# Kernel optimization log

Measured on AMD Instinct MI355X. Metric: run time of the kernel, lower is better.

## Reference

```python
import jax, jax.numpy as jnp
import numpy as np

B, T, D, H = 2, 2048, 1024, 16
HD = D // H  # head dim = 64; rope half-dim = 32


def setup_inputs() -> dict:
    key = jax.random.key(0)
    ks = jax.random.split(key, 8)
    x = jax.random.normal(ks[0], (B, T, D), dtype=jnp.float32)
    # additive causal mask (upper triangle = -inf-like), as typically passed in
    mask = jnp.triu(jnp.full((T, T), -1e9, dtype=jnp.float32), k=1)
    # standard RoPE angles: theta = pos / 10000^(2i/hd)
    inv_freq = 1.0 / (10000.0 ** (np.arange(0, HD, 2, dtype=np.float32) / HD))
    ang = np.arange(T, dtype=np.float32)[:, None] * inv_freq[None, :]  # [T, HD//2]
    cos = jnp.asarray(np.cos(ang), dtype=jnp.float32)
    sin = jnp.asarray(np.sin(ang), dtype=jnp.float32)
    s = 1.0 / np.sqrt(D)
    Wq = jax.random.normal(ks[1], (D, D), dtype=jnp.float32) * s
    bq = jnp.zeros((D,), dtype=jnp.float32)
    Wk = jax.random.normal(ks[2], (D, D), dtype=jnp.float32) * s
    Wv = jax.random.normal(ks[3], (D, D), dtype=jnp.float32) * s
    bv = jnp.zeros((D,), dtype=jnp.float32)
    Wo = jax.random.normal(ks[4], (D, D), dtype=jnp.float32) * s
    bo = jnp.zeros((D,), dtype=jnp.float32)
    return {"x": x, "mask": mask, "cos": cos, "sin": sin, "Wq": Wq, "bq": bq,
            "Wk": Wk, "Wv": Wv, "bv": bv, "Wo": Wo, "bo": bo}


def _apply_rope(t, cos, sin):
    # t: [B, T, H, HD]; cos/sin: [T, HD//2]; complex multiply on (even, odd) pairs
    t = t.reshape(B, T, H, HD // 2, 2)
    t0, t1 = t[..., 0], t[..., 1]
    c = cos[None, :, None, :]
    s = sin[None, :, None, :]
    out = jnp.stack([t0 * c - t1 * s, t0 * s + t1 * c], axis=-1)
    return out.reshape(B, T, H, HD)


def reference(x, mask, cos, sin, Wq, bq, Wk, Wv, bv, Wo, bo):
    scale = float(HD) ** (-0.25)
    q = (x @ Wq.T + bq).reshape(B, T, H, HD)
    k = (x @ Wk.T).reshape(B, T, H, HD)  # key proj has no bias
    v = (x @ Wv.T + bv).reshape(B, T, H, HD)
    q = _apply_rope(q, cos, sin)
    k = _apply_rope(k, cos, sin)
    q = q.transpose(0, 2, 1, 3) * scale  # [B,H,T,HD]
    k = k.transpose(0, 2, 1, 3) * scale
    v = v.transpose(0, 2, 1, 3)
    qk = jnp.einsum("bhtd,bhsd->bhts", q, k) + mask  # [B,H,T,T]
    qk = qk.astype(jnp.float32)
    w = jax.nn.softmax(qk, axis=-1).astype(q.dtype)
    wv = jnp.einsum("bhts,bhsd->bhtd", w, v)
    wv = wv.transpose(0, 2, 1, 3).reshape(B, T, D)
    out = wv @ Wo.T + bo
    return out, qk
```

## Files before the change

### kernel.cpp

```cpp
#include <hip/hip_runtime.h>
#include <math.h>

#define Tc 2048
#define Dc 1024
#define Hc 16
#define HDc 64
#define BT 4096
#define SCALE 0.35355339059327379f

typedef _Float16 f16;
typedef __attribute__((ext_vector_type(4))) _Float16 f16x4;
typedef __attribute__((ext_vector_type(8))) _Float16 f16x8;
typedef __attribute__((ext_vector_type(4))) float f32x4;

__device__ __forceinline__ void gload16(const f16* g, f16* l)
{
    __builtin_amdgcn_global_load_lds(
        (const __attribute__((address_space(1))) void*)g,
        (__attribute__((address_space(3))) void*)l, 16, 0, 0);
}

__global__ __launch_bounds__(256)
void cast_kernel(const float* __restrict__ x,
                 const float* __restrict__ Wq, const float* __restrict__ Wk,
                 const float* __restrict__ Wv, const float* __restrict__ Wo,
                 f16* __restrict__ xh,
                 f16* __restrict__ Wqh, f16* __restrict__ Wkh,
                 f16* __restrict__ Wvh, f16* __restrict__ Woh)
{
    const int u = blockIdx.y;
    const float* s; f16* d;
    if (u < 4) { s = x + (size_t)u * (1u << 20); d = xh + (size_t)u * (1u << 20); }
    else switch (u) {
        case 4:  s = Wq; d = Wqh; break;
        case 5:  s = Wk; d = Wkh; break;
        case 6:  s = Wv; d = Wvh; break;
        default: s = Wo; d = Woh; break;
    }
    int i = blockIdx.x * 256 + threadIdx.x;
    float4 v = ((const float4*)s)[i];
    f16x4 o = {(f16)v.x, (f16)v.y, (f16)v.z, (f16)v.w};
    ((f16x4*)d)[i] = o;
}

#define GEMM_BODY(Aptr, Bptr)                                                        \
    __shared__ f16 As[128][64];                                                      \
    __shared__ f16 Bs[128][64];                                                      \
    const int tid = threadIdx.x;                                                     \
    const int w = tid >> 6, l = tid & 63;                                            \
    const int lr = l & 15, lq = l >> 4;                                              \
    const int wr = w >> 1, wc = w & 1;                                               \
    const int m0 = blockIdx.y * 128, n0 = blockIdx.x * 128;                          \
    const int srow8 = l >> 3, sslot = l & 7;                                         \
    f32x4 acc[4][4] = {};                                                            \
    for (int k0 = 0; k0 < Dc; k0 += 64) {                                            \
        __syncthreads();                                                             \
        _Pragma("unroll")                                                            \
        for (int c = 0; c < 4; c++) {                                                \
            int chunk = w * 4 + c;                                                   \
            int row = chunk * 8 + srow8;                                             \
            int col = (sslot ^ (row & 7)) * 8;                                       \
            gload16(&Aptr[(size_t)(m0 + row) * Dc + k0 + col],                       \
                    (f16*)((char*)&As[0][0] + chunk * 1024));                        \
            gload16(&Bptr[(size_t)(n0 + row) * Dc + k0 + col],                       \
                    (f16*)((char*)&Bs[0][0] + chunk * 1024));                        \
        }                                                                            \
        __syncthreads();                                                             \
        _Pragma("unroll")                                                            \
        for (int kk = 0; kk < 2; kk++) {                                             \
            f16x8 af[4], bf[4];                                                      \
            _Pragma("unroll")                                                        \
            for (int mi = 0; mi < 4; mi++) {                                         \
                int row = 64 * wr + 16 * mi + lr;                                    \
                int bo = (lq * 16 + kk * 64) ^ ((row & 7) << 4);                     \
                af[mi] = *(const f16x8*)((const char*)&As[0][0] + row * 128 + bo);   \
            }                                                                        \
            _Pragma("unroll")                                                        \
            for (int ni = 0; ni < 4; ni++) {                                         \
                int row = 64 * wc + 16 * ni + lr;                                    \
                int bo = (lq * 16 + kk * 64) ^ ((row & 7) << 4);                     \
                bf[ni] = *(const f16x8*)((const char*)&Bs[0][0] + row * 128 + bo);   \
            }                                                                        \
            _Pragma("unroll")                                                        \
            for (int mi = 0; mi < 4; mi++)                                           \
                _Pragma("unroll")                                                    \
                for (int ni = 0; ni < 4; ni++)                                       \
                    acc[mi][ni] = __builtin_amdgcn_mfma_f32_16x16x32_f16(            \
                        af[mi], bf[ni], acc[mi][ni], 0, 0, 0);                       \
        }                                                                            \
    }

__global__ __launch_bounds__(256)
void qkv_proj_kernel(const f16* __restrict__ xh,
                     const f16* __restrict__ Wqh, const f16* __restrict__ Wkh,
                     const f16* __restrict__ Wvh,
                     const float* __restrict__ bq, const float* __restrict__ bv,
                     f16* __restrict__ qh, f16* __restrict__ kh, f16* __restrict__ vh,
                     const float* __restrict__ cosp, const float* __restrict__ sinp)
{
    const int mode = blockIdx.z;
    const f16* W = (mode == 0) ? Wqh : (mode == 1 ? Wkh : Wvh);
    const float* bias = (mode == 0) ? bq : (mode == 2 ? bv : nullptr);
    f16* dst = (mode == 0) ? qh : (mode == 1 ? kh : vh);

    GEMM_BODY(xh, W)

    #pragma unroll
    for (int mi = 0; mi < 4; mi++) {
        #pragma unroll
        for (int ni = 0; ni < 4; ni++) {
            #pragma unroll
            for (int i = 0; i < 4; i++) {
                int gm = m0 + 64 * wr + 16 * mi + lq * 4 + i;
                int gn = n0 + 64 * wc + 16 * ni + lr;
                float v = acc[mi][ni][i];
                if (bias) v += bias[gn];
                int b = gm >> 11, t = gm & 2047;
                int h = gn >> 6, d = gn & 63;
                if (mode != 2) {
                    float pv = __shfl_xor(v, 1, 64);
                    int p = d >> 1;
                    float c = cosp[t * 32 + p], s = sinp[t * 32 + p];
                    v = (d & 1) ? (pv * s + v * c) : (v * c - pv * s);
                    v *= SCALE;
                }
                dst[((size_t)(b * Hc + h) * Tc + t) * HDc + d] = (f16)v;
            }
        }
    }
}

__global__ __launch_bounds__(256)
void out_proj_kernel(const f16* __restrict__ A, const f16* __restrict__ W,
                     const float* __restrict__ bias, float* __restrict__ out)
{
    GEMM_BODY(A, W)

    #pragma unroll
    for (int mi = 0; mi < 4; mi++)
        #pragma unroll
        for (int ni = 0; ni < 4; ni++)
            #pragma unroll
            for (int i = 0; i < 4; i++) {
                int gm = m0 + 64 * wr + 16 * mi + lq * 4 + i;
                int gn = n0 + 64 * wc + 16 * ni + lr;
                out[(size_t)gm * Dc + gn] = acc[mi][ni][i] + bias[gn];
            }
}

__global__ __launch_bounds__(256)
void flash_kernel(const f16* __restrict__ qh, const f16* __restrict__ kh,
                  const f16* __restrict__ vh, f16* __restrict__ wvh,
                  float* __restrict__ qk)
{
    const int z = blockIdx.y;
    const int t0 = (gridDim.x - 1 - blockIdx.x) * 64;
    const int tid = threadIdx.x;
    const int w = tid >> 6, l = tid & 63;
    const int lr = l & 15, lq = l >> 4;

    __shared__ f16 Ks[64][72];
    __shared__ f16 VsT[64][72];
    __shared__ f16 Ps[64][72];

    const f16* Qg = qh + (size_t)z * Tc * HDc;
    const f16* Kg = kh + (size_t)z * Tc * HDc;
    const f16* Vg = vh + (size_t)z * Tc * HDc;
    float* C = qk + (size_t)z * Tc * Tc;

    f16x8 aq[2];
    #pragma unroll
    for (int ks = 0; ks < 2; ks++)
        aq[ks] = *(const f16x8*)&Qg[(size_t)(t0 + 16 * w + lr) * HDc + lq * 8 + 32 * ks];

    {
        int r = t0 + (tid >> 2);
        int n4 = (Tc - t0 - 64) >> 2;
        float4 mv; mv.x = mv.y = mv.z = mv.w = -1e9f;
        float4* rowp = (float4*)(C + (size_t)r * Tc + t0 + 64);
        for (int c = (tid & 3); c < n4; c += 4) rowp[c] = mv;
    }

    const int kr = tid >> 2, kc = (tid & 3) * 16;
    const int vs = tid & 63, vd = (tid >> 6) * 16;
    f16x8 rk0 = *(const f16x8*)&Kg[(size_t)kr * HDc + kc];
    f16x8 rk1 = *(const f16x8*)&Kg[(size_t)kr * HDc + kc + 8];
    f16x8 rv0 = *(const f16x8*)&Vg[(size_t)vs * HDc + vd];
    f16x8 rv1 = *(const f16x8*)&Vg[(size_t)vs * HDc + vd + 8];

    f32x4 O[4] = {};
    float mrow[4], lrow[4];
    #pragma unroll
    for (int i = 0; i < 4; i++) { mrow[i] = -1e30f; lrow[i] = 0.f; }

    for (int s0 = 0; s0 <= t0; s0 += 64) {
        asm volatile("" ::: "memory");
        __builtin_amdgcn_s_barrier();
        asm volatile("" ::: "memory");

        *(f16x8*)&Ks[kr][kc]     = rk0;
        *(f16x8*)&Ks[kr][kc + 8] = rk1;
        #pragma unroll
        for (int j = 0; j < 8; j++) {
            VsT[vd + j][vs]     = rv0[j];
            VsT[vd + 8 + j][vs] = rv1[j];
        }

        if (s0 + 64 <= t0) {
            const f16* kp = &Kg[(size_t)(s0 + 64 + kr) * HDc + kc];
            const f16* vp = &Vg[(size_t)(s0 + 64 + vs) * HDc + vd];
            rk0 = *(const f16x8*)kp;
            rk1 = *(const f16x8*)(kp + 8);
            rv0 = *(const f16x8*)vp;
            rv1 = *(const f16x8*)(vp + 8);
        }

        asm volatile("s_waitcnt lgkmcnt(0)" ::: "memory");
        __builtin_amdgcn_s_barrier();
        asm volatile("" ::: "memory");

        f32x4 S[4] = {};
        __builtin_amdgcn_s_setprio(1);
        #pragma unroll
        for (int ks = 0; ks < 2; ks++) {
            #pragma unroll
            for (int ni = 0; ni < 4; ni++) {
                f16x8 bk = *(const f16x8*)&Ks[16 * ni + lr][lq * 8 + 32 * ks];
                S[ni] = __builtin_amdgcn_mfma_f32_16x16x32_f16(aq[ks], bk, S[ni], 0, 0, 0);
            }
        }
        __builtin_amdgcn_s_setprio(0);

        if (s0 == t0) {
            #pragma unroll
            for (int ni = 0; ni < 4; ni++)
                #pragma unroll
                for (int i = 0; i < 4; i++) {
                    int tg = t0 + 16 * w + lq * 4 + i;
                    int sg = s0 + 16 * ni + lr;
                    if (sg > tg) S[ni][i] = -1e9f;
                }
        }

        #pragma unroll
        for (int ni = 0; ni < 4; ni++)
            #pragma unroll
            for (int i = 0; i < 4; i++) {
                int tg = t0 + 16 * w + lq * 4 + i;
                int sg = s0 + 16 * ni + lr;
                C[(size_t)tg * Tc + sg] = S[ni][i];
            }

        #pragma unroll
        for (int i = 0; i < 4; i++) {
            float v = fmaxf(fmaxf(S[0][i], S[1][i]), fmaxf(S[2][i], S[3][i]));
            v = fmaxf(v, __shfl_xor(v, 1, 64));
            v = fmaxf(v, __shfl_xor(v, 2, 64));
            v = fmaxf(v, __shfl_xor(v, 4, 64));
            v = fmaxf(v, __shfl_xor(v, 8, 64));
            float mnew = fmaxf(mrow[i], v);
            float alpha = __expf(mrow[i] - mnew);
            mrow[i] = mnew;
            float rs = 0.f;
            #pragma unroll
            for (int ni = 0; ni < 4; ni++) {
                float p = __expf(S[ni][i] - mnew);
                S[ni][i] = p;
                rs += p;
            }
            rs += __shfl_xor(rs, 1, 64);
            rs += __shfl_xor(rs, 2, 64);
            rs += __shfl_xor(rs, 4, 64);
            rs += __shfl_xor(rs, 8, 64);
            lrow[i] = lrow[i] * alpha + rs;
            #pragma unroll
            for (int ni = 0; ni < 4; ni++) O[ni][i] *= alpha;
        }

        #pragma unroll
        for (int ni = 0; ni < 4; ni++)
            #pragma unroll
            for (int i = 0; i < 4; i++)
                Ps[16 * w + lq * 4 + i][16 * ni + lr] = (f16)S[ni][i];

        __builtin_amdgcn_s_setprio(1);
        #pragma unroll
        for (int ks = 0; ks < 2; ks++) {
            f16x8 ap = *(const f16x8*)&Ps[16 * w + lr][lq * 8 + 32 * ks];
            #pragma unroll
            for (int ni = 0; ni < 4; ni++) {
                f16x8 bv = *(const f16x8*)&VsT[16 * ni + lr][lq * 8 + 32 * ks];
                O[ni] = __builtin_amdgcn_mfma_f32_16x16x32_f16(ap, bv, O[ni], 0, 0, 0);
            }
        }
        __builtin_amdgcn_s_setprio(0);
    }

    const int b = z >> 4, h = z & 15;
    #pragma unroll
    for (int ni = 0; ni < 4; ni++)
        #pragma unroll
        for (int i = 0; i < 4; i++) {
            int tg = t0 + 16 * w + lq * 4 + i;
            int d = 16 * ni + lr;
            float o = O[ni][i] / lrow[i];
            wvh[((size_t)(b * Tc + tg)) * Dc + h * HDc + d] = (f16)o;
        }
}

extern "C" void kernel_launch(void* const* d_in, const int* in_sizes, int n_in,
                              void* d_out, int out_size, void* d_ws, size_t ws_size,
                              hipStream_t stream)
{
    const float* x    = (const float*)d_in[0];
    const float* cosp = (const float*)d_in[2];
    const float* sinp = (const float*)d_in[3];
    const float* Wq   = (const float*)d_in[4];
    const float* bq   = (const float*)d_in[5];
    const float* Wk   = (const float*)d_in[6];
    const float* Wv   = (const float*)d_in[7];
    const float* bv   = (const float*)d_in[8];
    const float* Wo   = (const float*)d_in[9];
    const float* bo   = (const float*)d_in[10];

    float* out = (float*)d_out;
    float* qk  = out + (size_t)BT * Dc;

    f16* ws  = (f16*)d_ws;
    f16* xh  = ws;
    f16* Wqh = xh  + (size_t)BT * Dc;
    f16* Wkh = Wqh + (size_t)Dc * Dc;
    f16* Wvh = Wkh + (size_t)Dc * Dc;
    f16* Woh = Wvh + (size_t)Dc * Dc;
    f16* qh  = Woh + (size_t)Dc * Dc;
    f16* kh  = qh  + (size_t)BT * Dc;
    f16* vh  = kh  + (size_t)BT * Dc;
    f16* wvh = vh  + (size_t)BT * Dc;

    dim3 blk(256);

    cast_kernel<<<dim3(1024, 8), blk, 0, stream>>>(
        x, Wq, Wk, Wv, Wo, xh, Wqh, Wkh, Wvh, Woh);

    qkv_proj_kernel<<<dim3(Dc / 128, BT / 128, 3), blk, 0, stream>>>(
        xh, Wqh, Wkh, Wvh, bq, bv, qh, kh, vh, cosp, sinp);

    flash_kernel<<<dim3(Tc / 64, 32), blk, 0, stream>>>(qh, kh, vh, wvh, qk);

    out_proj_kernel<<<dim3(Dc / 128, BT / 128), blk, 0, stream>>>(wvh, Woh, bo, out);
}
```

Before: 781.8 us.

## Load K tiles directly to LDS with swizzle, drop register prefetch, raise occupancy

The flash kernel now streams K tiles straight from global memory into LDS using global_load_lds with an XOR-swizzled layout, instead of prefetching K and V into registers one iteration ahead. LDS padding shrinks (K unpadded and swizzled, V/P padded to 68) and launch bounds request 6 waves per SIMD. The aim is to cut register pressure and LDS footprint so more blocks fit per CU. In exchange, the software prefetch of the next tile is gone, so global load latency is now exposed within each iteration unless the higher occupancy hides it.

```diff
diff --git a/kernel.cpp b/kernel.cpp
--- a/kernel.cpp
+++ b/kernel.cpp
@@ -148,7 +148,7 @@
             }
 }
 
-__global__ __launch_bounds__(256)
+__global__ __launch_bounds__(256, 6)
 void flash_kernel(const f16* __restrict__ qh, const f16* __restrict__ kh,
                   const f16* __restrict__ vh, f16* __restrict__ wvh,
                   float* __restrict__ qk)
@@ -159,9 +159,9 @@
     const int w = tid >> 6, l = tid & 63;
     const int lr = l & 15, lq = l >> 4;
 
-    __shared__ f16 Ks[64][72];
-    __shared__ f16 VsT[64][72];
-    __shared__ f16 Ps[64][72];
+    __shared__ f16 Ks[64][64];
+    __shared__ f16 VsT[64][68];
+    __shared__ f16 Ps[64][68];
 
     const f16* Qg = qh + (size_t)z * Tc * HDc;
     const f16* Kg = kh + (size_t)z * Tc * HDc;
@@ -181,43 +181,35 @@
         for (int c = (tid & 3); c < n4; c += 4) rowp[c] = mv;
     }
 
-    const int kr = tid >> 2, kc = (tid & 3) * 16;
-    const int vs = tid & 63, vd = (tid >> 6) * 16;
-    f16x8 rk0 = *(const f16x8*)&Kg[(size_t)kr * HDc + kc];
-    f16x8 rk1 = *(const f16x8*)&Kg[(size_t)kr * HDc + kc + 8];
-    f16x8 rv0 = *(const f16x8*)&Vg[(size_t)vs * HDc + vd];
-    f16x8 rv1 = *(const f16x8*)&Vg[(size_t)vs * HDc + vd + 8];
-
     f32x4 O[4] = {};
     float mrow[4], lrow[4];
     #pragma unroll
     for (int i = 0; i < 4; i++) { mrow[i] = -1e30f; lrow[i] = 0.f; }
 
+    const int srow8 = l >> 3, sslot = l & 7;
+
     for (int s0 = 0; s0 <= t0; s0 += 64) {
-        asm volatile("" ::: "memory");
-        __builtin_amdgcn_s_barrier();
-        asm volatile("" ::: "memory");
-
-        *(f16x8*)&Ks[kr][kc]     = rk0;
-        *(f16x8*)&Ks[kr][kc + 8] = rk1;
-        #pragma unroll
-        for (int j = 0; j < 8; j++) {
-            VsT[vd + j][vs]     = rv0[j];
-            VsT[vd + 8 + j][vs] = rv1[j];
-        }
-
-        if (s0 + 64 <= t0) {
-            const f16* kp = &Kg[(size_t)(s0 + 64 + kr) * HDc + kc];
-            const f16* vp = &Vg[(size_t)(s0 + 64 + vs) * HDc + vd];
-            rk0 = *(const f16x8*)kp;
-            rk1 = *(const f16x8*)(kp + 8);
-            rv0 = *(const f16x8*)vp;
-            rv1 = *(const f16x8*)(vp + 8);
-        }
-
-        asm volatile("s_waitcnt lgkmcnt(0)" ::: "memory");
-        __builtin_amdgcn_s_barrier();
-        asm volatile("" ::: "memory");
+        __syncthreads();
+
+        #pragma unroll
+        for (int c = 0; c < 2; c++) {
+            int chunk = w * 2 + c;
+            int row = chunk * 8 + srow8;
+            int col = (sslot ^ (row & 7)) * 8;
+            gload16(&Kg[(size_t)(s0 + row) * HDc + col],
+                    (f16*)((char*)&Ks[0][0] + chunk * 1024));
+        }
+        {
+            const f16* vp = &Vg[(size_t)(s0 + l) * HDc + w * 16];
+            f16x8 v0 = *(const f16x8*)vp;
+            f16x8 v1 = *(const f16x8*)(vp + 8);
+            #pragma unroll
+            for (int j = 0; j < 8; j++) {
+                VsT[w * 16 + j][l]     = v0[j];
+                VsT[w * 16 + 8 + j][l] = v1[j];
+            }
+        }
+        __syncthreads();
 
         f32x4 S[4] = {};
         __builtin_amdgcn_s_setprio(1);
@@ -225,7 +217,9 @@
         for (int ks = 0; ks < 2; ks++) {
             #pragma unroll
             for (int ni = 0; ni < 4; ni++) {
-                f16x8 bk = *(const f16x8*)&Ks[16 * ni + lr][lq * 8 + 32 * ks];
+                int krow = 16 * ni + lr;
+                int bo = (lq * 16 + ks * 64) ^ ((krow & 7) << 4);
+                f16x8 bk = *(const f16x8*)((const char*)&Ks[0][0] + krow * 128 + bo);
                 S[ni] = __builtin_amdgcn_mfma_f32_16x16x32_f16(aq[ks], bk, S[ni], 0, 0, 0);
             }
         }
```

After: 767.4 us. Within noise of the previous version (-1.8%).
